# Optimization experiments

Measured on AMD Instinct MI355X. Metric: run time of the kernel, lower is better.

## Reference

```python
import jax, jax.numpy as jnp
import numpy as np

N = 131072
IN_C1 = 64
MED_C = 64
OUT_C = 64
EPS = 1e-8


def _glorot(key, shape):
    fan_in = shape[0]
    bound = 1.0 / np.sqrt(fan_in)
    return jax.random.uniform(key, shape, jnp.float32, -bound, bound)


def setup_inputs() -> dict:
    key = jax.random.key(0)
    ks = jax.random.split(key, 16)
    inp = {
        "key_value_input": jax.random.normal(ks[0], (N, IN_C1), jnp.float32),
        "query_input": jax.random.normal(ks[1], (N, 7), jnp.float32),
        # Linear params stored as [in, out] (y = x @ W + b)
        "key_W": _glorot(ks[2], (IN_C1, MED_C)), "key_b": jnp.zeros((MED_C,), jnp.float32),
        "value_W": _glorot(ks[3], (IN_C1, MED_C)), "value_b": jnp.zeros((MED_C,), jnp.float32),
        "T_W": _glorot(ks[4], (7, MED_C * MED_C)), "T_b": jnp.zeros((MED_C * MED_C,), jnp.float32),
        "d1_W": _glorot(ks[5], (MED_C, 64)), "d1_b": jnp.zeros((64,), jnp.float32),
        "d2_W": _glorot(ks[6], (64, 32)), "d2_b": jnp.zeros((32,), jnp.float32),
        "d3_W": _glorot(ks[7], (32, OUT_C)), "d3_b": jnp.zeros((OUT_C,), jnp.float32),
        "scale": jnp.float32(1.0),
    }
    return inp


def reference(key_value_input, query_input, key_W, key_b, value_W, value_b,
              T_W, T_b, d1_W, d1_b, d2_W, d2_b, d3_W, d3_b, scale):
    # Per-token hypernetwork: T [N, med_c, med_c]
    T = (query_input @ T_W + T_b).reshape(-1, MED_C, MED_C)
    k = key_value_input @ key_W + key_b              # [N, med_c]
    v = key_value_input @ value_W + value_b          # [N, med_c]
    # query = T @ kv  (batched mat-vec)
    q = jnp.einsum('nij,nj->ni', T, key_value_input)  # [N, med_c]
    att = q * k
    # F.normalize(p=2, dim=-1, eps=1e-8): x / max(||x||_2, eps)
    norm = jnp.linalg.norm(att, axis=-1, keepdims=True)
    att = att / jnp.maximum(norm, EPS)
    v = jax.nn.softmax(v * scale, axis=-1)
    x = att * v
    # small MLP head d
    h = jax.nn.relu(x @ d1_W + d1_b)
    h = jax.nn.relu(h @ d2_W + d2_b)
    return h @ d3_W + d3_b
```

## Files before the change

kernel.cpp:

```cpp
#include <hip/hip_runtime.h>
#include <math.h>

typedef _Float16 f16_t;
typedef __attribute__((ext_vector_type(8))) _Float16 f16x8;
typedef __attribute__((ext_vector_type(4))) float f32x4;

#define NTOK 131072
#define MT   64
#define TPB  128
#define RP16 72
#define OP32 68
#define SLABB 4608

#define OFF_KEY 0
#define OFF_VAL 4096
#define OFF_T   8192
#define OFF_D1  40960
#define OFF_D2  45056
#define OFF_D3  47104
#define WTOT    49152

__device__ __forceinline__ f32x4 mfma1(f16x8 a, f16x8 b, f32x4 c) {
    return __builtin_amdgcn_mfma_f32_16x16x32_f16(a, b, c, 0, 0, 0);
}

#define DPPF(x, C) __int_as_float(__builtin_amdgcn_update_dpp( \
    0, __float_as_int(x), (C), 0xF, 0xF, true))

__device__ __forceinline__ void red16_sum4(f32x4& x) {
#pragma unroll
    for (int e = 0; e < 4; ++e) {
        float v = x[e];
        v += DPPF(v, 0xB1);
        v += DPPF(v, 0x4E);
        v += DPPF(v, 0x141);
        v += DPPF(v, 0x140);
        x[e] = v;
    }
}
__device__ __forceinline__ void red16_max4(f32x4& x) {
#pragma unroll
    for (int e = 0; e < 4; ++e) {
        float v = x[e];
        v = fmaxf(v, DPPF(v, 0xB1));
        v = fmaxf(v, DPPF(v, 0x4E));
        v = fmaxf(v, DPPF(v, 0x141));
        v = fmaxf(v, DPPF(v, 0x140));
        x[e] = v;
    }
}

struct B2 { f16x8 b0, b1; };

__device__ __forceinline__ B2 loadB_lds(const f16_t* __restrict__ b, int c, int l15, int quad) {
    const char* base = (const char*)b;
    int o0 = (16 * c + l15) * 128 + quad * 16;
    int sw = (l15 & 7) << 4;
    B2 r;
    r.b0 = *(const f16x8*)(base + (o0 ^ sw));
    r.b1 = *(const f16x8*)(base + ((o0 + 64) ^ sw));
    return r;
}

#define GEMML(buf, c, a00, a01, a10, a11, acc0, acc1) do {        \
    B2 Bf = loadB_lds((buf), (c), l15, quad);                      \
    acc0 = mfma1(a01, Bf.b1, mfma1(a00, Bf.b0, acc0));             \
    acc1 = mfma1(a11, Bf.b1, mfma1(a10, Bf.b0, acc1));             \
} while (0)

__device__ __forceinline__ void gl_lds16(const void* g, void* l) {
    __builtin_amdgcn_global_load_lds(
        (const __attribute__((address_space(1))) unsigned int*)g,
        (__attribute__((address_space(3))) unsigned int*)l, 16, 0, 0);
}

__device__ __forceinline__ void stage8k(const f16_t* __restrict__ gsrc, f16_t* lbuf, int tid) {
#pragma unroll
    for (int i = 0; i < 4; ++i) {
        int o = (i * TPB + tid) * 16;
        int g = o ^ (((o >> 7) & 7) << 4);
        gl_lds16((const char*)gsrc + g, (char*)lbuf + (o & ~1023));
    }
}
__device__ __forceinline__ void stage4k_r128(const f16_t* __restrict__ gsrc, f16_t* lbuf, int tid) {
#pragma unroll
    for (int i = 0; i < 2; ++i) {
        int o = (i * TPB + tid) * 16;
        int g = o ^ (((o >> 7) & 7) << 4);
        gl_lds16((const char*)gsrc + g, (char*)lbuf + (o & ~1023));
    }
}
__device__ __forceinline__ void stage4k_r64(const f16_t* __restrict__ gsrc, f16_t* lbuf, int tid) {
#pragma unroll
    for (int i = 0; i < 2; ++i) {
        int o = (i * TPB + tid) * 16;
        int g = o ^ (((o >> 7) & 3) << 4);
        gl_lds16((const char*)gsrc + g, (char*)lbuf + (o & ~1023));
    }
}

#define VMW4() asm volatile("s_waitcnt vmcnt(4)" ::: "memory")
#define VMW0() asm volatile("s_waitcnt vmcnt(0)" ::: "memory")
#define BAR()  do { __builtin_amdgcn_s_barrier(); asm volatile("" ::: "memory"); } while (0)
#define BARREL() do { asm volatile("s_waitcnt lgkmcnt(0)" ::: "memory"); \
                      __builtin_amdgcn_s_barrier(); \
                      asm volatile("" ::: "memory"); } while (0)

__global__ __launch_bounds__(256)
void prep_w(const float* __restrict__ keyW, const float* __restrict__ valW,
            const float* __restrict__ TW,   const float* __restrict__ TB,
            const float* __restrict__ d1W,  const float* __restrict__ d2W,
            const float* __restrict__ d3W,  f16_t* __restrict__ wsf)
{
    int idx = blockIdx.x * 256 + threadIdx.x;
    if (idx >= WTOT) return;
    float src;
    if (idx < OFF_VAL) {
        int r = idx - OFF_KEY, n = r >> 6, j = r & 63;
        src = keyW[j * 64 + n];
    } else if (idx < OFF_T) {
        int r = idx - OFF_VAL, n = r >> 6, j = r & 63;
        src = valW[j * 64 + n];
    } else if (idx < OFF_D1) {
        int r = idx - OFF_T, p = r >> 12, q = r & 4095;
        src = (p < 7) ? TW[p * 4096 + q] : TB[q];
    } else if (idx < OFF_D2) {
        int r = idx - OFF_D1, n = r >> 6, j = r & 63;
        src = d1W[j * 64 + n];
    } else if (idx < OFF_D3) {
        int r = idx - OFF_D2, n = r >> 6, j = r & 63;
        src = d2W[j * 32 + n];
    } else {
        int r = idx - OFF_D3, n = r >> 5, j = r & 31;
        src = d3W[j * 64 + n];
    }
    wsf[idx] = (f16_t)src;
}

__device__ __forceinline__ void front_rt(
    f16_t* __restrict__ Rf,
    const f16_t* __restrict__ keyb, const f16_t* __restrict__ valb,
    int l15, int quad, int rtb,
    f16x8 a0, f16x8 a1,
    f32x4 q0, f32x4 q1, f32x4 q2, f32x4 q3,
    f32x4 kbv, f32x4 vbv, float sc)
{
    f32x4 k0 = {}, k1 = {}, k2 = {}, k3 = {}, v0 = {}, v1 = {}, v2 = {}, v3 = {};
    { B2 B = loadB_lds(keyb, 0, l15, quad); k0 = mfma1(a1, B.b1, mfma1(a0, B.b0, k0)); }
    { B2 B = loadB_lds(keyb, 1, l15, quad); k1 = mfma1(a1, B.b1, mfma1(a0, B.b0, k1)); }
    { B2 B = loadB_lds(keyb, 2, l15, quad); k2 = mfma1(a1, B.b1, mfma1(a0, B.b0, k2)); }
    { B2 B = loadB_lds(keyb, 3, l15, quad); k3 = mfma1(a1, B.b1, mfma1(a0, B.b0, k3)); }
    { B2 B = loadB_lds(valb, 0, l15, quad); v0 = mfma1(a1, B.b1, mfma1(a0, B.b0, v0)); }
    { B2 B = loadB_lds(valb, 1, l15, quad); v1 = mfma1(a1, B.b1, mfma1(a0, B.b0, v1)); }
    { B2 B = loadB_lds(valb, 2, l15, quad); v2 = mfma1(a1, B.b1, mfma1(a0, B.b0, v2)); }
    { B2 B = loadB_lds(valb, 3, l15, quad); v3 = mfma1(a1, B.b1, mfma1(a0, B.b0, v3)); }

    f32x4 sv0 = (v0 + vbv[0]) * sc;
    f32x4 sv1 = (v1 + vbv[1]) * sc;
    f32x4 sv2 = (v2 + vbv[2]) * sc;
    f32x4 sv3 = (v3 + vbv[3]) * sc;

    f32x4 mx;
#pragma unroll
    for (int e = 0; e < 4; ++e)
        mx[e] = fmaxf(fmaxf(sv0[e], sv1[e]), fmaxf(sv2[e], sv3[e]));
    red16_max4(mx);
#pragma unroll
    for (int e = 0; e < 4; ++e) {
        sv0[e] = __expf(sv0[e] - mx[e]);
        sv1[e] = __expf(sv1[e] - mx[e]);
        sv2[e] = __expf(sv2[e] - mx[e]);
        sv3[e] = __expf(sv3[e] - mx[e]);
    }
    f32x4 se = sv0 + sv1 + sv2 + sv3;
    red16_sum4(se);

    f32x4 at0 = q0 * (k0 + kbv[0]);
    f32x4 at1 = q1 * (k1 + kbv[1]);
    f32x4 at2 = q2 * (k2 + kbv[2]);
    f32x4 at3 = q3 * (k3 + kbv[3]);
    f32x4 nr = at0 * at0 + at1 * at1 + at2 * at2 + at3 * at3;
    red16_sum4(nr);

    f32x4 fac;
#pragma unroll
    for (int e = 0; e < 4; ++e)
        fac[e] = 1.0f / (fmaxf(sqrtf(nr[e]), 1e-8f) * se[e]);

#pragma unroll
    for (int e = 0; e < 4; ++e) {
        f16_t* rr = Rf + (rtb + quad * 4 + e) * RP16 + l15;
        rr[0]  = (f16_t)(at0[e] * sv0[e] * fac[e]);
        rr[16] = (f16_t)(at1[e] * sv1[e] * fac[e]);
        rr[32] = (f16_t)(at2[e] * sv2[e] * fac[e]);
        rr[48] = (f16_t)(at3[e] * sv3[e] * fac[e]);
    }
}

__device__ __forceinline__ void d1_rt(f16_t* __restrict__ Rf, const f16_t* __restrict__ wb,
                                      int l15, int quad, int rtb, f32x4 b1v)
{
    f16x8 x00 = *(const f16x8*)(Rf + (rtb + l15) * RP16 + quad * 8);
    f16x8 x01 = *(const f16x8*)(Rf + (rtb + l15) * RP16 + 32 + quad * 8);
    f16x8 x10 = *(const f16x8*)(Rf + (rtb + 16 + l15) * RP16 + quad * 8);
    f16x8 x11 = *(const f16x8*)(Rf + (rtb + 16 + l15) * RP16 + 32 + quad * 8);
    f32x4 h00 = {}, h01 = {}, h02 = {}, h03 = {};
    f32x4 h10 = {}, h11 = {}, h12 = {}, h13 = {};
    GEMML(wb, 0, x00, x01, x10, x11, h00, h10);
    GEMML(wb, 1, x00, x01, x10, x11, h01, h11);
    GEMML(wb, 2, x00, x01, x10, x11, h02, h12);
    GEMML(wb, 3, x00, x01, x10, x11, h03, h13);
#pragma unroll
    for (int e = 0; e < 4; ++e) {
        f16_t* r0 = Rf + (rtb + quad * 4 + e) * RP16 + l15;
        r0[0]  = (f16_t)fmaxf(h00[e] + b1v[0], 0.f);
        r0[16] = (f16_t)fmaxf(h01[e] + b1v[1], 0.f);
        r0[32] = (f16_t)fmaxf(h02[e] + b1v[2], 0.f);
        r0[48] = (f16_t)fmaxf(h03[e] + b1v[3], 0.f);
        f16_t* r1 = Rf + (rtb + 16 + quad * 4 + e) * RP16 + l15;
        r1[0]  = (f16_t)fmaxf(h10[e] + b1v[0], 0.f);
        r1[16] = (f16_t)fmaxf(h11[e] + b1v[1], 0.f);
        r1[32] = (f16_t)fmaxf(h12[e] + b1v[2], 0.f);
        r1[48] = (f16_t)fmaxf(h13[e] + b1v[3], 0.f);
    }
}

__device__ __forceinline__ void d2_rt(f16_t* __restrict__ Rf, const f16_t* __restrict__ wb,
                                      int l15, int quad, int rtb, float b20, float b21)
{
    f16x8 x00 = *(const f16x8*)(Rf + (rtb + l15) * RP16 + quad * 8);
    f16x8 x01 = *(const f16x8*)(Rf + (rtb + l15) * RP16 + 32 + quad * 8);
    f16x8 x10 = *(const f16x8*)(Rf + (rtb + 16 + l15) * RP16 + quad * 8);
    f16x8 x11 = *(const f16x8*)(Rf + (rtb + 16 + l15) * RP16 + 32 + quad * 8);
    f32x4 g00 = {}, g01 = {}, g10 = {}, g11 = {};
    GEMML(wb, 0, x00, x01, x10, x11, g00, g10);
    GEMML(wb, 1, x00, x01, x10, x11, g01, g11);
#pragma unroll
    for (int e = 0; e < 4; ++e) {
        f16_t* r0 = Rf + (rtb + quad * 4 + e) * RP16 + l15;
        r0[0]  = (f16_t)fmaxf(g00[e] + b20, 0.f);
        r0[16] = (f16_t)fmaxf(g01[e] + b21, 0.f);
        f16_t* r1 = Rf + (rtb + 16 + quad * 4 + e) * RP16 + l15;
        r1[0]  = (f16_t)fmaxf(g10[e] + b20, 0.f);
        r1[16] = (f16_t)fmaxf(g11[e] + b21, 0.f);
    }
}

__device__ __forceinline__ void d3_rt(f16_t* __restrict__ Rf, float* __restrict__ Of,
                                      const char* __restrict__ d3b,
                                      int l15, int quad, int lane, int rtb,
                                      f32x4 b3v, float* __restrict__ obase)
{
    f16x8 a30 = *(const f16x8*)(Rf + (rtb + l15) * RP16 + quad * 8);
    f16x8 a31 = *(const f16x8*)(Rf + (rtb + 16 + l15) * RP16 + quad * 8);
    const int sw3 = ((l15 >> 1) & 3) << 4;
#pragma unroll
    for (int h = 0; h < 2; ++h) {
        const f16x8 a3 = h ? a31 : a30;
#pragma unroll
        for (int c = 0; c < 4; ++c) {
            int o3 = (16 * c + l15) * 64 + quad * 16;
            f16x8 bw = *(const f16x8*)(d3b + (o3 ^ sw3));
            f32x4 z = {};
            f32x4 o = mfma1(a3, bw, z);
#pragma unroll
            for (int e = 0; e < 4; ++e)
                Of[(quad * 4 + e) * OP32 + 16 * c + l15] = o[e] + b3v[c];
        }
#pragma unroll
        for (int i = 0; i < 4; ++i) {
            const int r4 = i * 4 + quad;
            f32x4 v = *(const f32x4*)(Of + r4 * OP32 + l15 * 4);
            *(f32x4*)(obase + rtb * 64 + h * 1024 + i * 256 + lane * 4) = v;
        }
    }
}

__global__ __launch_bounds__(TPB, 2)
void fused_mfma(const float* __restrict__ kv_in, const float* __restrict__ q_in,
                const float* __restrict__ keyB,  const float* __restrict__ valB,
                const float* __restrict__ d1B,   const float* __restrict__ d2B,
                const float* __restrict__ d3B,   const float* __restrict__ scale_p,
                const f16_t* __restrict__ wsf,   float* __restrict__ out)
{
    __shared__ __align__(16) unsigned char Slab[2][SLABB];
    __shared__ __align__(16) f16_t Qs16[MT][8];
    __shared__ __align__(16) f16_t WB[2][4096];

    const int tid  = threadIdx.x;
    const int wv   = tid >> 6, lane = tid & 63;
    const int quad = lane >> 4, l15 = lane & 15;
    const int RB   = wv * 32;
    const long t0  = (long)blockIdx.x * MT;

    f16_t* __restrict__ Rf = (f16_t*)Slab[wv];
    float* __restrict__ Of = (float*)Slab[wv];

    {
        const int r = lane >> 1, half = lane & 1;
        const float4* p4 = (const float4*)(kv_in + (t0 + RB + r) * 64 + half * 32);
        f16_t* dst = Rf + r * RP16 + half * 32;
#pragma unroll
        for (int b = 0; b < 4; ++b) {
            float4 f0 = p4[2 * b], f1 = p4[2 * b + 1];
            f16x8 h;
            h[0] = (f16_t)f0.x; h[1] = (f16_t)f0.y; h[2] = (f16_t)f0.z; h[3] = (f16_t)f0.w;
            h[4] = (f16_t)f1.x; h[5] = (f16_t)f1.y; h[6] = (f16_t)f1.z; h[7] = (f16_t)f1.w;
            *(f16x8*)(dst + 8 * b) = h;
        }
    }
    if (lane < 32) {
        const float* qp = q_in + (t0 + RB + lane) * 7;
        f16x8 qh;
#pragma unroll
        for (int p = 0; p < 7; ++p) qh[p] = (f16_t)qp[p];
        qh[7] = (f16_t)1.0f;
        *(f16x8*)&Qs16[RB + lane][0] = qh;
    }
    f32x4 kbv, vbv, b1v, b3v;
#pragma unroll
    for (int c = 0; c < 4; ++c) {
        kbv[c] = keyB[16 * c + l15];  vbv[c] = valB[16 * c + l15];
        b1v[c] = d1B[16 * c + l15];   b3v[c] = d3B[16 * c + l15];
    }
    const float b20 = d2B[l15], b21 = d2B[16 + l15];
    const float sc = scale_p[0];

    stage8k(wsf + OFF_T + 0 * 4096, WB[0], tid);
    stage8k(wsf + OFF_T + 1 * 4096, WB[1], tid);

    f16x8 ah00 = *(const f16x8*)(Rf + l15 * RP16 + quad * 8);
    f16x8 ah01 = *(const f16x8*)(Rf + l15 * RP16 + 32 + quad * 8);
    f16x8 ah10 = *(const f16x8*)(Rf + (16 + l15) * RP16 + quad * 8);
    f16x8 ah11 = *(const f16x8*)(Rf + (16 + l15) * RP16 + 32 + quad * 8);

    f32x4 q00 = {}, q01 = {}, q02 = {}, q03 = {};
    f32x4 q10 = {}, q11 = {}, q12 = {}, q13 = {};
#pragma unroll 1
    for (int p = 0; p < 8; ++p) {
        const f16_t* tb = WB[p & 1];
        VMW4(); BAR();
        f16_t s0 = Qs16[RB + l15][p];
        f16_t s1 = Qs16[RB + 16 + l15][p];
        f16x8 w0 = {s0, s0, s0, s0, s0, s0, s0, s0};
        f16x8 w1 = {s1, s1, s1, s1, s1, s1, s1, s1};
        f16x8 sa00 = ah00 * w0, sa01 = ah01 * w0;
        f16x8 sa10 = ah10 * w1, sa11 = ah11 * w1;
        { B2 B = loadB_lds(tb, 0, l15, quad);
          q00 = mfma1(sa01, B.b1, mfma1(sa00, B.b0, q00));
          q10 = mfma1(sa11, B.b1, mfma1(sa10, B.b0, q10)); }
        { B2 B = loadB_lds(tb, 1, l15, quad);
          q01 = mfma1(sa01, B.b1, mfma1(sa00, B.b0, q01));
          q11 = mfma1(sa11, B.b1, mfma1(sa10, B.b0, q11)); }
        { B2 B = loadB_lds(tb, 2, l15, quad);
          q02 = mfma1(sa01, B.b1, mfma1(sa00, B.b0, q02));
          q12 = mfma1(sa11, B.b1, mfma1(sa10, B.b0, q12)); }
        { B2 B = loadB_lds(tb, 3, l15, quad);
          q03 = mfma1(sa01, B.b1, mfma1(sa00, B.b0, q03));
          q13 = mfma1(sa11, B.b1, mfma1(sa10, B.b0, q13)); }
        BARREL();
        const f16_t* nsrc = (p < 6) ? (wsf + OFF_T + (p + 2) * 4096)
                                    : ((p == 6) ? (wsf + OFF_KEY) : (wsf + OFF_VAL));
        stage8k(nsrc, WB[p & 1], tid);
    }
    VMW0(); BAR();

    front_rt(Rf, WB[0], WB[1], l15, quad, 0,  ah00, ah01, q00, q01, q02, q03, kbv, vbv, sc);
    front_rt(Rf, WB[0], WB[1], l15, quad, 16, ah10, ah11, q10, q11, q12, q13, kbv, vbv, sc);
    BARREL();
    stage8k(wsf + OFF_D1, WB[0], tid);
    stage4k_r128(wsf + OFF_D2, WB[1], tid);
    stage4k_r64 (wsf + OFF_D3, WB[1] + 2048, tid);
    VMW0(); BAR();

    d1_rt(Rf, WB[0], l15, quad, 0, b1v);
    d2_rt(Rf, WB[1], l15, quad, 0, b20, b21);

    float* __restrict__ obase = out + (t0 + RB) * 64;
    const char* d3b = (const char*)(&WB[1][2048]);
    d3_rt(Rf, Of, d3b, l15, quad, lane, 0, b3v, obase);
}

extern "C" void kernel_launch(void* const* d_in, const int* in_sizes, int n_in,
                              void* d_out, int out_size, void* d_ws, size_t ws_size,
                              hipStream_t stream) {
    (void)in_sizes; (void)n_in; (void)out_size; (void)ws_size;
    const float* kv_in = (const float*)d_in[0];
    const float* q_in  = (const float*)d_in[1];
    const float* keyW  = (const float*)d_in[2];
    const float* keyB  = (const float*)d_in[3];
    const float* valW  = (const float*)d_in[4];
    const float* valB  = (const float*)d_in[5];
    const float* TW    = (const float*)d_in[6];
    const float* TB    = (const float*)d_in[7];
    const float* d1W   = (const float*)d_in[8];
    const float* d1B   = (const float*)d_in[9];
    const float* d2W   = (const float*)d_in[10];
    const float* d2B   = (const float*)d_in[11];
    const float* d3W   = (const float*)d_in[12];
    const float* d3B   = (const float*)d_in[13];
    const float* scale = (const float*)d_in[14];
    f16_t* wsf = (f16_t*)d_ws;
    float* outp = (float*)d_out;

    prep_w<<<(WTOT + 255) / 256, 256, 0, stream>>>(keyW, valW, TW, TB, d1W, d2W, d3W, wsf);
    fused_mfma<<<NTOK / MT, TPB, 0, stream>>>(kv_in, q_in, keyB, valB,
                                              d1B, d2B, d3B, scale, wsf, outp);
}
```

Before: 135.8 us.

## Stage all weights in LDS once per block and loop over two token tiles

Switches from 128-thread blocks that stream T/key/value/MLP weights through double-buffered LDS per 64-token tile to 512-thread blocks that load all 96KB of fp16 weights into LDS once. Each block then processes two 256-token tiles, prefetching the next tile's inputs into registers while computing. The per-phase barriers and restaging are removed, and weight traffic is amortised over more tokens. The cost is far more LDS per block (about 133KB), which limits occupancy to one block per CU. It also delays the start of work until the whole weight set is staged.

```diff
diff --git a/kernel.cpp b/kernel.cpp
--- a/kernel.cpp
+++ b/kernel.cpp
@@ -5,11 +5,13 @@
 typedef __attribute__((ext_vector_type(8))) _Float16 f16x8;
 typedef __attribute__((ext_vector_type(4))) float f32x4;
 
-#define NTOK 131072
-#define MT   64
-#define TPB  128
-#define RP16 72
-#define OP32 68
+#define NTOK  131072
+#define MT    256
+#define TPB   512
+#define TILES 2
+#define NBLK  (NTOK / (MT * TILES))
+#define RP16  72
+#define OP32  68
 #define SLABB 4608
 
 #define OFF_KEY 0
@@ -74,37 +76,26 @@
         (__attribute__((address_space(3))) unsigned int*)l, 16, 0, 0);
 }
 
-__device__ __forceinline__ void stage8k(const f16_t* __restrict__ gsrc, f16_t* lbuf, int tid) {
-#pragma unroll
-    for (int i = 0; i < 4; ++i) {
-        int o = (i * TPB + tid) * 16;
-        int g = o ^ (((o >> 7) & 7) << 4);
-        gl_lds16((const char*)gsrc + g, (char*)lbuf + (o & ~1023));
-    }
-}
-__device__ __forceinline__ void stage4k_r128(const f16_t* __restrict__ gsrc, f16_t* lbuf, int tid) {
-#pragma unroll
-    for (int i = 0; i < 2; ++i) {
-        int o = (i * TPB + tid) * 16;
-        int g = o ^ (((o >> 7) & 7) << 4);
-        gl_lds16((const char*)gsrc + g, (char*)lbuf + (o & ~1023));
-    }
-}
-__device__ __forceinline__ void stage4k_r64(const f16_t* __restrict__ gsrc, f16_t* lbuf, int tid) {
-#pragma unroll
-    for (int i = 0; i < 2; ++i) {
-        int o = (i * TPB + tid) * 16;
+__device__ __forceinline__ void stage_all(const f16_t* __restrict__ wsf,
+                                          f16_t* Wl, int tid) {
+#pragma unroll
+    for (int i = 0; i < 12; ++i) {
+        int idx = i * TPB + tid;
+        if (idx < 5888) {
+            int o = idx * 16;
+            int g = o ^ (((o >> 7) & 7) << 4);
+            gl_lds16((const char*)wsf + g, (char*)Wl + (o & ~1023));
+        }
+    }
+    if (tid < 256) {
+        int o = tid * 16;
         int g = o ^ (((o >> 7) & 3) << 4);
-        gl_lds16((const char*)gsrc + g, (char*)lbuf + (o & ~1023));
-    }
-}
-
-#define VMW4() asm volatile("s_waitcnt vmcnt(4)" ::: "memory")
+        gl_lds16((const char*)wsf + 94208 + g, (char*)Wl + 94208 + (o & ~1023));
+    }
+}
+
 #define VMW0() asm volatile("s_waitcnt vmcnt(0)" ::: "memory")
 #define BAR()  do { __builtin_amdgcn_s_barrier(); asm volatile("" ::: "memory"); } while (0)
-#define BARREL() do { asm volatile("s_waitcnt lgkmcnt(0)" ::: "memory"); \
-                      __builtin_amdgcn_s_barrier(); \
-                      asm volatile("" ::: "memory"); } while (0)
 
 __global__ __launch_bounds__(256)
 void prep_w(const float* __restrict__ keyW, const float* __restrict__ valW,
@@ -283,40 +274,31 @@
                 const float* __restrict__ d3B,   const float* __restrict__ scale_p,
                 const f16_t* __restrict__ wsf,   float* __restrict__ out)
 {
-    __shared__ __align__(16) unsigned char Slab[2][SLABB];
-    __shared__ __align__(16) f16_t Qs16[MT][8];
-    __shared__ __align__(16) f16_t WB[2][4096];
+    __shared__ __align__(16) f16_t Wlds[WTOT];
+    __shared__ __align__(16) unsigned char Slab[8][SLABB];
+    __shared__ __align__(16) f16_t Qs16[8][32][8];
 
     const int tid  = threadIdx.x;
     const int wv   = tid >> 6, lane = tid & 63;
     const int quad = lane >> 4, l15 = lane & 15;
-    const int RB   = wv * 32;
-    const long t0  = (long)blockIdx.x * MT;
+    const long t0  = (long)blockIdx.x * (MT * TILES);
 
     f16_t* __restrict__ Rf = (f16_t*)Slab[wv];
     float* __restrict__ Of = (float*)Slab[wv];
-
-    {
-        const int r = lane >> 1, half = lane & 1;
-        const float4* p4 = (const float4*)(kv_in + (t0 + RB + r) * 64 + half * 32);
-        f16_t* dst = Rf + r * RP16 + half * 32;
-#pragma unroll
-        for (int b = 0; b < 4; ++b) {
-            float4 f0 = p4[2 * b], f1 = p4[2 * b + 1];
-            f16x8 h;
-            h[0] = (f16_t)f0.x; h[1] = (f16_t)f0.y; h[2] = (f16_t)f0.z; h[3] = (f16_t)f0.w;
-            h[4] = (f16_t)f1.x; h[5] = (f16_t)f1.y; h[6] = (f16_t)f1.z; h[7] = (f16_t)f1.w;
-            *(f16x8*)(dst + 8 * b) = h;
-        }
-    }
+    const int r = lane >> 1, half = lane & 1;
+
+    const float4* p40 = (const float4*)(kv_in + (t0 + wv * 32 + r) * 64 + half * 32);
+    float4 kf0 = p40[0], kf1 = p40[1], kf2 = p40[2], kf3 = p40[3],
+           kf4 = p40[4], kf5 = p40[5], kf6 = p40[6], kf7 = p40[7];
+    float qv0 = 0, qv1 = 0, qv2 = 0, qv3 = 0, qv4 = 0, qv5 = 0, qv6 = 0;
     if (lane < 32) {
-        const float* qp = q_in + (t0 + RB + lane) * 7;
-        f16x8 qh;
-#pragma unroll
-        for (int p = 0; p < 7; ++p) qh[p] = (f16_t)qp[p];
-        qh[7] = (f16_t)1.0f;
-        *(f16x8*)&Qs16[RB + lane][0] = qh;
-    }
+        const float* qp = q_in + (t0 + wv * 32 + lane) * 7;
+        qv0 = qp[0]; qv1 = qp[1]; qv2 = qp[2]; qv3 = qp[3];
+        qv4 = qp[4]; qv5 = qp[5]; qv6 = qp[6];
+    }
+
+    stage_all(wsf, Wlds, tid);
+
     f32x4 kbv, vbv, b1v, b3v;
 #pragma unroll
     for (int c = 0; c < 4; ++c) {
@@ -326,59 +308,87 @@
     const float b20 = d2B[l15], b21 = d2B[16 + l15];
     const float sc = scale_p[0];
 
-    stage8k(wsf + OFF_T + 0 * 4096, WB[0], tid);
-    stage8k(wsf + OFF_T + 1 * 4096, WB[1], tid);
-
-    f16x8 ah00 = *(const f16x8*)(Rf + l15 * RP16 + quad * 8);
-    f16x8 ah01 = *(const f16x8*)(Rf + l15 * RP16 + 32 + quad * 8);
-    f16x8 ah10 = *(const f16x8*)(Rf + (16 + l15) * RP16 + quad * 8);
-    f16x8 ah11 = *(const f16x8*)(Rf + (16 + l15) * RP16 + 32 + quad * 8);
-
-    f32x4 q00 = {}, q01 = {}, q02 = {}, q03 = {};
-    f32x4 q10 = {}, q11 = {}, q12 = {}, q13 = {};
+    const f16_t* KEYp = Wlds + OFF_KEY;
+    const f16_t* VALp = Wlds + OFF_VAL;
+    const f16_t* D1p  = Wlds + OFF_D1;
+    const f16_t* D2p  = Wlds + OFF_D2;
+    const char*  d3b  = (const char*)(Wlds + OFF_D3);
+
 #pragma unroll 1
-    for (int p = 0; p < 8; ++p) {
-        const f16_t* tb = WB[p & 1];
-        VMW4(); BAR();
-        f16_t s0 = Qs16[RB + l15][p];
-        f16_t s1 = Qs16[RB + 16 + l15][p];
-        f16x8 w0 = {s0, s0, s0, s0, s0, s0, s0, s0};
-        f16x8 w1 = {s1, s1, s1, s1, s1, s1, s1, s1};
-        f16x8 sa00 = ah00 * w0, sa01 = ah01 * w0;
-        f16x8 sa10 = ah10 * w1, sa11 = ah11 * w1;
-        { B2 B = loadB_lds(tb, 0, l15, quad);
-          q00 = mfma1(sa01, B.b1, mfma1(sa00, B.b0, q00));
-          q10 = mfma1(sa11, B.b1, mfma1(sa10, B.b0, q10)); }
-        { B2 B = loadB_lds(tb, 1, l15, quad);
-          q01 = mfma1(sa01, B.b1, mfma1(sa00, B.b0, q01));
-          q11 = mfma1(sa11, B.b1, mfma1(sa10, B.b0, q11)); }
-        { B2 B = loadB_lds(tb, 2, l15, quad);
-          q02 = mfma1(sa01, B.b1, mfma1(sa00, B.b0, q02));
-          q12 = mfma1(sa11, B.b1, mfma1(sa10, B.b0, q12)); }
-        { B2 B = loadB_lds(tb, 3, l15, quad);
-          q03 = mfma1(sa01, B.b1, mfma1(sa00, B.b0, q03));
-          q13 = mfma1(sa11, B.b1, mfma1(sa10, B.b0, q13)); }
-        BARREL();
-        const f16_t* nsrc = (p < 6) ? (wsf + OFF_T + (p + 2) * 4096)
-                                    : ((p == 6) ? (wsf + OFF_KEY) : (wsf + OFF_VAL));
-        stage8k(nsrc, WB[p & 1], tid);
-    }
-    VMW0(); BAR();
-
-    front_rt(Rf, WB[0], WB[1], l15, quad, 0,  ah00, ah01, q00, q01, q02, q03, kbv, vbv, sc);
-    front_rt(Rf, WB[0], WB[1], l15, quad, 16, ah10, ah11, q10, q11, q12, q13, kbv, vbv, sc);
-    BARREL();
-    stage8k(wsf + OFF_D1, WB[0], tid);
-    stage4k_r128(wsf + OFF_D2, WB[1], tid);
-    stage4k_r64 (wsf + OFF_D3, WB[1] + 2048, tid);
-    VMW0(); BAR();
-
-    d1_rt(Rf, WB[0], l15, quad, 0, b1v);
-    d2_rt(Rf, WB[1], l15, quad, 0, b20, b21);
-
-    float* __restrict__ obase = out + (t0 + RB) * 64;
-    const char* d3b = (const char*)(&WB[1][2048]);
-    d3_rt(Rf, Of, d3b, l15, quad, lane, 0, b3v, obase);
+    for (int t = 0; t < TILES; ++t) {
+        {
+            f16_t* dst = Rf + r * RP16 + half * 32;
+            f16x8 h;
+            h[0]=(f16_t)kf0.x; h[1]=(f16_t)kf0.y; h[2]=(f16_t)kf0.z; h[3]=(f16_t)kf0.w;
+            h[4]=(f16_t)kf1.x; h[5]=(f16_t)kf1.y; h[6]=(f16_t)kf1.z; h[7]=(f16_t)kf1.w;
+            *(f16x8*)(dst + 0) = h;
+            h[0]=(f16_t)kf2.x; h[1]=(f16_t)kf2.y; h[2]=(f16_t)kf2.z; h[3]=(f16_t)kf2.w;
+            h[4]=(f16_t)kf3.x; h[5]=(f16_t)kf3.y; h[6]=(f16_t)kf3.z; h[7]=(f16_t)kf3.w;
+            *(f16x8*)(dst + 8) = h;
+            h[0]=(f16_t)kf4.x; h[1]=(f16_t)kf4.y; h[2]=(f16_t)kf4.z; h[3]=(f16_t)kf4.w;
+            h[4]=(f16_t)kf5.x; h[5]=(f16_t)kf5.y; h[6]=(f16_t)kf5.z; h[7]=(f16_t)kf5.w;
+            *(f16x8*)(dst + 16) = h;
+            h[0]=(f16_t)kf6.x; h[1]=(f16_t)kf6.y; h[2]=(f16_t)kf6.z; h[3]=(f16_t)kf6.w;
+            h[4]=(f16_t)kf7.x; h[5]=(f16_t)kf7.y; h[6]=(f16_t)kf7.z; h[7]=(f16_t)kf7.w;
+            *(f16x8*)(dst + 24) = h;
+        }
+        if (lane < 32) {
+            f16x8 qh;
+            qh[0]=(f16_t)qv0; qh[1]=(f16_t)qv1; qh[2]=(f16_t)qv2; qh[3]=(f16_t)qv3;
+            qh[4]=(f16_t)qv4; qh[5]=(f16_t)qv5; qh[6]=(f16_t)qv6; qh[7]=(f16_t)1.0f;
+            *(f16x8*)&Qs16[wv][lane][0] = qh;
+        }
+        f16x8 ah00 = *(const f16x8*)(Rf + l15 * RP16 + quad * 8);
+        f16x8 ah01 = *(const f16x8*)(Rf + l15 * RP16 + 32 + quad * 8);
+        f16x8 ah10 = *(const f16x8*)(Rf + (16 + l15) * RP16 + quad * 8);
+        f16x8 ah11 = *(const f16x8*)(Rf + (16 + l15) * RP16 + 32 + quad * 8);
+
+        if (t == 0) { VMW0(); BAR(); }
+
+        if (t + 1 < TILES) {
+            const float4* pn = (const float4*)(kv_in + (t0 + (t + 1) * MT + wv * 32 + r) * 64 + half * 32);
+            kf0 = pn[0]; kf1 = pn[1]; kf2 = pn[2]; kf3 = pn[3];
+            kf4 = pn[4]; kf5 = pn[5]; kf6 = pn[6]; kf7 = pn[7];
+            if (lane < 32) {
+                const float* qp = q_in + (t0 + (t + 1) * MT + wv * 32 + lane) * 7;
+                qv0 = qp[0]; qv1 = qp[1]; qv2 = qp[2]; qv3 = qp[3];
+                qv4 = qp[4]; qv5 = qp[5]; qv6 = qp[6];
+            }
+        }
+
+        f32x4 q00 = {}, q01 = {}, q02 = {}, q03 = {};
+        f32x4 q10 = {}, q11 = {}, q12 = {}, q13 = {};
+#pragma unroll 1
+        for (int p = 0; p < 8; ++p) {
+            const f16_t* tb = Wlds + OFF_T + p * 4096;
+            f16_t s0 = Qs16[wv][l15][p];
+            f16_t s1 = Qs16[wv][16 + l15][p];
+            f16x8 w0 = {s0, s0, s0, s0, s0, s0, s0, s0};
+            f16x8 w1 = {s1, s1, s1, s1, s1, s1, s1, s1};
+            f16x8 sa00 = ah00 * w0, sa01 = ah01 * w0;
+            f16x8 sa10 = ah10 * w1, sa11 = ah11 * w1;
+            { B2 B = loadB_lds(tb, 0, l15, quad);
+              q00 = mfma1(sa01, B.b1, mfma1(sa00, B.b0, q00));
+              q10 = mfma1(sa11, B.b1, mfma1(sa10, B.b0, q10)); }
+            { B2 B = loadB_lds(tb, 1, l15, quad);
+              q01 = mfma1(sa01, B.b1, mfma1(sa00, B.b0, q01));
+              q11 = mfma1(sa11, B.b1, mfma1(sa10, B.b0, q11)); }
+            { B2 B = loadB_lds(tb, 2, l15, quad);
+              q02 = mfma1(sa01, B.b1, mfma1(sa00, B.b0, q02));
+              q12 = mfma1(sa11, B.b1, mfma1(sa10, B.b0, q12)); }
+            { B2 B = loadB_lds(tb, 3, l15, quad);
+              q03 = mfma1(sa01, B.b1, mfma1(sa00, B.b0, q03));
+              q13 = mfma1(sa11, B.b1, mfma1(sa10, B.b0, q13)); }
+        }
+
+        front_rt(Rf, KEYp, VALp, l15, quad, 0,  ah00, ah01, q00, q01, q02, q03, kbv, vbv, sc);
+        front_rt(Rf, KEYp, VALp, l15, quad, 16, ah10, ah11, q10, q11, q12, q13, kbv, vbv, sc);
+
+        d1_rt(Rf, D1p, l15, quad, 0, b1v);
+        d2_rt(Rf, D2p, l15, quad, 0, b20, b21);
+        float* __restrict__ obase = out + (t0 + t * MT + wv * 32) * 64;
+        d3_rt(Rf, Of, d3b, l15, quad, lane, 0, b3v, obase);
+    }
 }
 
 extern "C" void kernel_launch(void* const* d_in, const int* in_sizes, int n_in,
@@ -404,6 +414,6 @@
     float* outp = (float*)d_out;
 
     prep_w<<<(WTOT + 255) / 256, 256, 0, stream>>>(keyW, valW, TW, TB, d1W, d2W, d3W, wsf);
-    fused_mfma<<<NTOK / MT, TPB, 0, stream>>>(kv_in, q_in, keyB, valB,
-                                              d1B, d2B, d3B, scale, wsf, outp);
-}
+    fused_mfma<<<NBLK, TPB, 0, stream>>>(kv_in, q_in, keyB, valB,
+                                         d1B, d2B, d3B, scale, wsf, outp);
+}
```

Measured after the change: 134.7 us. Within noise of the previous version (-0.8%).
